# Kernel optimization log

Measured on AMD Instinct MI355X. Metric: run time of the kernel, lower is better.

## Reference

```python
import jax, jax.numpy as jnp
import numpy as np

B = 64
D = 4096          # width of every layer
# DAG: layer k consumes concat of prior layer outputs listed here (0 = input x)
CONNECTIONS = {1: [0], 2: [0, 1], 3: [1, 2], 4: [2, 3]}


def setup_inputs() -> dict:
    key = jax.random.key(0)
    keys = iter(jax.random.split(key, 32))
    inp = {"x": jax.random.normal(next(keys), (B, D), dtype=jnp.float32)}
    for k, v in CONNECTIONS.items():
        fan_in = D * len(v)
        bound = 1.0 / np.sqrt(fan_in)
        # kaiming_uniform_(a=sqrt(5)) -> U(-sqrt(6/((1+5)*fan_in)), +) = U(-1/sqrt(fan_in), +)
        inp[f"W{k}"] = jax.random.uniform(next(keys), (D, fan_in), jnp.float32, -bound, bound)
        inp[f"b{k}"] = jax.random.uniform(next(keys), (D,), jnp.float32, -bound, bound)
        # static binary mask (buffer in torch), stored as float like MaskedLinear expects
        inp[f"M{k}"] = (jax.random.uniform(next(keys), (D, fan_in)) < 0.5).astype(jnp.float32)
    return inp


def _dag_forward(x, Ws, bs, Ms):
    layer_output = [x]
    for k, v in CONNECTIONS.items():
        inputs = jnp.concatenate([layer_output[v_] for v_ in v], axis=1)  # [B, D*len(v)]
        # masked linear: y = inputs @ (W*M)^T + b, then ReLU
        y = jnp.einsum('bi,oi->bo', inputs, Ws[k] * Ms[k]) + bs[k]
        layer_output.append(jax.nn.relu(y))
    return layer_output[-1]


def reference(x, W1, b1, M1, W2, b2, M2, W3, b3, M3, W4, b4, M4):
    Ws = {1: W1, 2: W2, 3: W3, 4: W4}
    bs = {1: b1, 2: b2, 3: b3, 4: b4}
    Ms = {1: M1, 2: M2, 3: M3, 4: M4}
    return _dag_forward(x, Ws, bs, Ms)
```

## Files before the change

kernel.cpp:

```cpp
#include <hip/hip_runtime.h>
#include <hip/hip_bf16.h>
#include <stdint.h>


typedef __attribute__((ext_vector_type(8))) short  s8v;
typedef __attribute__((ext_vector_type(4))) float  f4v;
typedef __attribute__((ext_vector_type(2))) float  f2v;
typedef __attribute__((ext_vector_type(4))) unsigned short us4v;
typedef __attribute__((ext_vector_type(2))) unsigned short us2v;

#define LDA 16384
#define MFMA16 __builtin_amdgcn_mfma_f32_16x16x32_bf16

__device__ __forceinline__ short f2bf(float f) {
  unsigned int u = __builtin_bit_cast(unsigned int, f);
  u += 0x7fffu + ((u >> 16) & 1u);
  return (short)(u >> 16);
}
__device__ __forceinline__ float bf2f(short s) {
  unsigned int u = ((unsigned int)(unsigned short)s) << 16;
  return __builtin_bit_cast(float, u);
}

__global__ void dag_splitx(const float* __restrict__ x,
                           ushort* __restrict__ xh, ushort* __restrict__ xl) {
  int idx = blockIdx.x * blockDim.x + threadIdx.x;
  int m = idx >> 10;
  int n = (idx & 1023) << 2;
  f4v v = *(const f4v*)(x + (size_t)m * 4096 + n);
  us4v h, l;
#pragma unroll
  for (int j = 0; j < 4; ++j) {
    short hh = f2bf(v[j]);
    h[j] = (unsigned short)hh;
    l[j] = (unsigned short)f2bf(v[j] - bf2f(hh));
  }
  *(us4v*)(xh + (size_t)m * LDA + n) = h;
  *(us4v*)(xl + (size_t)m * LDA + n) = l;
}

struct RW { f4v w0a, w0b, w1a, w1b, m0a, m0b, m1a, m1b; };
struct RA { s8v ah0, ah1, ah2, ah3, al0, al1, al2, al3; };

template <int NSTEPS>
__global__ __launch_bounds__(256, 2) void dag_gemm_phaseA(
    const ushort* __restrict__ Ah,
    const ushort* __restrict__ Al,
    const float*  __restrict__ W,
    const float*  __restrict__ Mm,
    float*        __restrict__ partial,
    int K) {
  const int klen = NSTEPS * 32;
  const int tid  = threadIdx.x;
  const int wave = tid >> 6, lane = tid & 63;
  const int l15  = lane & 15, blk = lane >> 4;
  const int n0   = blockIdx.x * 128 + wave * 32;
  const int kbeg = blockIdx.y * klen;

  const float* wp0 = W  + (size_t)(n0 + l15) * K + kbeg + blk * 8;
  const float* wp1 = wp0 + (size_t)16 * K;
  const float* mp0 = Mm + (size_t)(n0 + l15) * K + kbeg + blk * 8;
  const float* mp1 = mp0 + (size_t)16 * K;
  const ushort* ap  = Ah + (size_t)l15 * LDA + kbeg + blk * 8;
  const ushort* alp = Al + (size_t)l15 * LDA + kbeg + blk * 8;

  f4v acc[4][2];
#pragma unroll
  for (int i = 0; i < 4; ++i) {
    acc[i][0] = (f4v){0.f, 0.f, 0.f, 0.f};
    acc[i][1] = (f4v){0.f, 0.f, 0.f, 0.f};
  }

  RW w[3];
  RA a[2];

  auto LOADW = [&](RW& r, int ko) {
    r.w0a = *(const f4v*)(wp0 + ko);     r.w0b = *(const f4v*)(wp0 + ko + 4);
    r.w1a = *(const f4v*)(wp1 + ko);     r.w1b = *(const f4v*)(wp1 + ko + 4);
    r.m0a = *(const f4v*)(mp0 + ko);     r.m0b = *(const f4v*)(mp0 + ko + 4);
    r.m1a = *(const f4v*)(mp1 + ko);     r.m1b = *(const f4v*)(mp1 + ko + 4);
  };
  auto LOADA = [&](RA& r, int ko) {
    r.ah0 = *(const s8v*)(ap  + ko);
    r.ah1 = *(const s8v*)(ap  + (size_t)16 * LDA + ko);
    r.ah2 = *(const s8v*)(ap  + (size_t)32 * LDA + ko);
    r.ah3 = *(const s8v*)(ap  + (size_t)48 * LDA + ko);
    r.al0 = *(const s8v*)(alp + ko);
    r.al1 = *(const s8v*)(alp + (size_t)16 * LDA + ko);
    r.al2 = *(const s8v*)(alp + (size_t)32 * LDA + ko);
    r.al3 = *(const s8v*)(alp + (size_t)48 * LDA + ko);
  };

  auto STEP = [&](RW& rw, RA& ra) {
    s8v wh0, wl0, wh1, wl1;
#pragma unroll
    for (int j = 0; j < 4; ++j) {
      { float ww = rw.w0a[j] * rw.m0a[j]; short h = f2bf(ww);
        wh0[j]     = h; wl0[j]     = f2bf(ww - bf2f(h)); }
      { float ww = rw.w0b[j] * rw.m0b[j]; short h = f2bf(ww);
        wh0[j + 4] = h; wl0[j + 4] = f2bf(ww - bf2f(h)); }
      { float ww = rw.w1a[j] * rw.m1a[j]; short h = f2bf(ww);
        wh1[j]     = h; wl1[j]     = f2bf(ww - bf2f(h)); }
      { float ww = rw.w1b[j] * rw.m1b[j]; short h = f2bf(ww);
        wh1[j + 4] = h; wl1[j + 4] = f2bf(ww - bf2f(h)); }
    }
    acc[0][0] = MFMA16(ra.ah0, wh0, acc[0][0], 0, 0, 0);
    acc[0][0] = MFMA16(ra.al0, wh0, acc[0][0], 0, 0, 0);
    acc[0][0] = MFMA16(ra.ah0, wl0, acc[0][0], 0, 0, 0);
    acc[1][0] = MFMA16(ra.ah1, wh0, acc[1][0], 0, 0, 0);
    acc[1][0] = MFMA16(ra.al1, wh0, acc[1][0], 0, 0, 0);
    acc[1][0] = MFMA16(ra.ah1, wl0, acc[1][0], 0, 0, 0);
    acc[2][0] = MFMA16(ra.ah2, wh0, acc[2][0], 0, 0, 0);
    acc[2][0] = MFMA16(ra.al2, wh0, acc[2][0], 0, 0, 0);
    acc[2][0] = MFMA16(ra.ah2, wl0, acc[2][0], 0, 0, 0);
    acc[3][0] = MFMA16(ra.ah3, wh0, acc[3][0], 0, 0, 0);
    acc[3][0] = MFMA16(ra.al3, wh0, acc[3][0], 0, 0, 0);
    acc[3][0] = MFMA16(ra.ah3, wl0, acc[3][0], 0, 0, 0);
    acc[0][1] = MFMA16(ra.ah0, wh1, acc[0][1], 0, 0, 0);
    acc[0][1] = MFMA16(ra.al0, wh1, acc[0][1], 0, 0, 0);
    acc[0][1] = MFMA16(ra.ah0, wl1, acc[0][1], 0, 0, 0);
    acc[1][1] = MFMA16(ra.ah1, wh1, acc[1][1], 0, 0, 0);
    acc[1][1] = MFMA16(ra.al1, wh1, acc[1][1], 0, 0, 0);
    acc[1][1] = MFMA16(ra.ah1, wl1, acc[1][1], 0, 0, 0);
    acc[2][1] = MFMA16(ra.ah2, wh1, acc[2][1], 0, 0, 0);
    acc[2][1] = MFMA16(ra.al2, wh1, acc[2][1], 0, 0, 0);
    acc[2][1] = MFMA16(ra.ah2, wl1, acc[2][1], 0, 0, 0);
    acc[3][1] = MFMA16(ra.ah3, wh1, acc[3][1], 0, 0, 0);
    acc[3][1] = MFMA16(ra.al3, wh1, acc[3][1], 0, 0, 0);
    acc[3][1] = MFMA16(ra.ah3, wl1, acc[3][1], 0, 0, 0);
  };

  LOADW(w[0], 0);
  if (NSTEPS > 1) LOADW(w[1], 32);
  LOADA(a[0], 0);
  if (NSTEPS > 1) LOADA(a[1], 32);

#pragma unroll
  for (int s = 0; s < NSTEPS; ++s) {
    if (s + 2 < NSTEPS) LOADW(w[(s + 2) % 3], (s + 2) * 32);
    STEP(w[s % 3], a[s & 1]);
    if (s + 2 < NSTEPS) LOADA(a[s & 1], (s + 2) * 32);
  }

  float* pout = partial + (size_t)blockIdx.y * (64 * 4096);
#pragma unroll
  for (int mt = 0; mt < 4; ++mt)
#pragma unroll
    for (int nt = 0; nt < 2; ++nt) {
      int n = n0 + nt * 16 + l15;
#pragma unroll
      for (int rr = 0; rr < 4; ++rr) {
        int m = mt * 16 + blk * 4 + rr;
        pout[(size_t)m * 4096 + n] = acc[mt][nt][rr];
      }
    }
}

__global__ void dag_phaseB(const float* __restrict__ partial, int splitk,
                           const float* __restrict__ bias,
                           ushort* __restrict__ yh, ushort* __restrict__ yl,
                           float* __restrict__ yf) {
  int idx = blockIdx.x * blockDim.x + threadIdx.x;
  int m = idx >> 11;
  int n = (idx & 2047) << 1;
  const float* p = partial + (size_t)m * 4096 + n;
  float s0 = 0.f, s1 = 0.f;
#pragma unroll 4
  for (int sp = 0; sp < splitk; ++sp) {
    f2v v = *(const f2v*)(p + (size_t)sp * (64 * 4096));
    s0 += v[0]; s1 += v[1];
  }
  const f2v bv = *(const f2v*)(bias + n);
  s0 = fmaxf(s0 + bv[0], 0.f);
  s1 = fmaxf(s1 + bv[1], 0.f);
  if (yf) {
    *(f2v*)(yf + (size_t)m * 4096 + n) = (f2v){s0, s1};
  } else {
    us2v h, l;
    short h0 = f2bf(s0); h[0] = (unsigned short)h0;
    l[0] = (unsigned short)f2bf(s0 - bf2f(h0));
    short h1 = f2bf(s1); h[1] = (unsigned short)h1;
    l[1] = (unsigned short)f2bf(s1 - bf2f(h1));
    *(us2v*)(yh + (size_t)m * LDA + n) = h;
    *(us2v*)(yl + (size_t)m * LDA + n) = l;
  }
}

extern "C" void kernel_launch(void* const* d_in, const int* in_sizes, int n_in,
                              void* d_out, int out_size, void* d_ws, size_t ws_size,
                              hipStream_t stream) {
  (void)in_sizes; (void)n_in; (void)out_size;
  const float* x = (const float*)d_in[0];
  struct L { const float *W, *b, *M; int K, incol, outcol; };
  L Ls[4] = {
      {(const float*)d_in[1],  (const float*)d_in[2],  (const float*)d_in[3],  4096, 0,    4096},
      {(const float*)d_in[4],  (const float*)d_in[5],  (const float*)d_in[6],  8192, 0,    8192},
      {(const float*)d_in[7],  (const float*)d_in[8],  (const float*)d_in[9],  8192, 4096, 12288},
      {(const float*)d_in[10], (const float*)d_in[11], (const float*)d_in[12], 8192, 8192, 16384},
  };
  float* out = (float*)d_out;

  char* ws = (char*)d_ws;
  ushort* Ah = (ushort*)ws;
  ushort* Al = (ushort*)(ws + (size_t)64 * LDA * 2);
  float* partial = (float*)(ws + (size_t)2 * 64 * LDA * 2);
  int SPLITK = 16;
  while (SPLITK > 1 &&
         ws_size < (size_t)4 * 1024 * 1024 + (size_t)SPLITK * 1024 * 1024)
    SPLITK >>= 1;

  dag_splitx<<<256, 256, 0, stream>>>(x, Ah, Al);

  for (int k = 0; k < 4; ++k) {
    dim3 grid(32, SPLITK);
    const ushort* Ahp = Ah + Ls[k].incol;
    const ushort* Alp = Al + Ls[k].incol;
    int nsteps = (Ls[k].K / SPLITK) / 32;
    switch (nsteps) {
      case 8:
        dag_gemm_phaseA<8><<<grid, 256, 0, stream>>>(
            Ahp, Alp, Ls[k].W, Ls[k].M, partial, Ls[k].K);
        break;
      case 16:
        dag_gemm_phaseA<16><<<grid, 256, 0, stream>>>(
            Ahp, Alp, Ls[k].W, Ls[k].M, partial, Ls[k].K);
        break;
      default:
        dag_gemm_phaseA<32><<<grid, 256, 0, stream>>>(
            Ahp, Alp, Ls[k].W, Ls[k].M, partial, Ls[k].K);
        break;
    }
    bool last = (k == 3);
    dag_phaseB<<<512, 256, 0, stream>>>(
        partial, SPLITK, Ls[k].b,
        last ? (ushort*)nullptr : Ah + Ls[k].outcol,
        last ? (ushort*)nullptr : Al + Ls[k].outcol,
        last ? out : (float*)nullptr);
  }
}
```

Measured before the change: 297.9 us.

## Stage weight and mask tiles through swizzled LDS with wider coalesced row loads

Weights and masks are no longer read straight into MFMA operand registers. Each wave now loads a 32-row by 64-column tile with 16 lanes covering one contiguous 256-byte row segment, writes it to a per-wave XOR-swizzled LDS region, and reads the MFMA fragments back from LDS. The aim is better global coalescing on the fp32 W and M streams, which dominate traffic. In exchange it adds LDS write and read traffic and 64 KB of dynamic shared memory per block, and the minimum split-K is raised to 4.

Result: faster. 280.9 us (-5.7%).

```diff
diff --git a/kernel.cpp b/kernel.cpp
--- a/kernel.cpp
+++ b/kernel.cpp
@@ -39,10 +39,9 @@
   *(us4v*)(xl + (size_t)m * LDA + n) = l;
 }
 
-struct RW { f4v w0a, w0b, w1a, w1b, m0a, m0b, m1a, m1b; };
 struct RA { s8v ah0, ah1, ah2, ah3, al0, al1, al2, al3; };
 
-template <int NSTEPS>
+template <int NSUPER>
 __global__ __launch_bounds__(256, 2) void dag_gemm_phaseA(
     const ushort* __restrict__ Ah,
     const ushort* __restrict__ Al,
@@ -50,35 +49,50 @@
     const float*  __restrict__ Mm,
     float*        __restrict__ partial,
     int K) {
-  const int klen = NSTEPS * 32;
+  extern __shared__ float smem[];
   const int tid  = threadIdx.x;
   const int wave = tid >> 6, lane = tid & 63;
   const int l15  = lane & 15, blk = lane >> 4;
   const int n0   = blockIdx.x * 128 + wave * 32;
+  const int klen = NSUPER * 64;
   const int kbeg = blockIdx.y * klen;
 
-  const float* wp0 = W  + (size_t)(n0 + l15) * K + kbeg + blk * 8;
-  const float* wp1 = wp0 + (size_t)16 * K;
-  const float* mp0 = Mm + (size_t)(n0 + l15) * K + kbeg + blk * 8;
-  const float* mp1 = mp0 + (size_t)16 * K;
+  float* WL = smem + wave * 4096;
+  float* ML = WL + 2048;
+
+  const int srow = lane >> 4;
+  const int sc   = lane & 15;
+
   const ushort* ap  = Ah + (size_t)l15 * LDA + kbeg + blk * 8;
   const ushort* alp = Al + (size_t)l15 * LDA + kbeg + blk * 8;
 
+  f4v stW[8], stM[8];
   f4v acc[4][2];
 #pragma unroll
   for (int i = 0; i < 4; ++i) {
     acc[i][0] = (f4v){0.f, 0.f, 0.f, 0.f};
     acc[i][1] = (f4v){0.f, 0.f, 0.f, 0.f};
   }
-
-  RW w[3];
-  RA a[2];
-
-  auto LOADW = [&](RW& r, int ko) {
-    r.w0a = *(const f4v*)(wp0 + ko);     r.w0b = *(const f4v*)(wp0 + ko + 4);
-    r.w1a = *(const f4v*)(wp1 + ko);     r.w1b = *(const f4v*)(wp1 + ko + 4);
-    r.m0a = *(const f4v*)(mp0 + ko);     r.m0b = *(const f4v*)(mp0 + ko + 4);
-    r.m1a = *(const f4v*)(mp1 + ko);     r.m1b = *(const f4v*)(mp1 + ko + 4);
+  RA a0, a1;
+
+  auto GLOAD = [&](int s) {
+    const float* wb = W  + (size_t)n0 * K + kbeg + s * 64 + sc * 4;
+    const float* mb = Mm + (size_t)n0 * K + kbeg + s * 64 + sc * 4;
+#pragma unroll
+    for (int j = 0; j < 8; ++j) {
+      size_t ro = (size_t)(4 * j + srow) * K;
+      stW[j] = *(const f4v*)(wb + ro);
+      stM[j] = *(const f4v*)(mb + ro);
+    }
+  };
+  auto DSWRITE = [&]() {
+#pragma unroll
+    for (int j = 0; j < 8; ++j) {
+      int row = 4 * j + srow;
+      int ci  = sc ^ (row & 15);
+      *(f4v*)(WL + row * 64 + ci * 4) = stW[j];
+      *(f4v*)(ML + row * 64 + ci * 4) = stM[j];
+    }
   };
   auto LOADA = [&](RA& r, int ko) {
     r.ah0 = *(const s8v*)(ap  + ko);
@@ -91,17 +105,28 @@
     r.al3 = *(const s8v*)(alp + (size_t)48 * LDA + ko);
   };
 
-  auto STEP = [&](RW& rw, RA& ra) {
+  auto KSTEP = [&](int kstep, RA& ra) {
+    const int cc = kstep * 8 + blk * 2;
+    const int c0 = cc ^ l15, c1 = (cc + 1) ^ l15;
+    const float* wr0 = WL + l15 * 64;
+    const float* wr1 = WL + (l15 + 16) * 64;
+    const float* mr0 = ML + l15 * 64;
+    const float* mr1 = ML + (l15 + 16) * 64;
+    f4v w0a = *(const f4v*)(wr0 + c0 * 4), w0b = *(const f4v*)(wr0 + c1 * 4);
+    f4v w1a = *(const f4v*)(wr1 + c0 * 4), w1b = *(const f4v*)(wr1 + c1 * 4);
+    f4v m0a = *(const f4v*)(mr0 + c0 * 4), m0b = *(const f4v*)(mr0 + c1 * 4);
+    f4v m1a = *(const f4v*)(mr1 + c0 * 4), m1b = *(const f4v*)(mr1 + c1 * 4);
+
     s8v wh0, wl0, wh1, wl1;
 #pragma unroll
     for (int j = 0; j < 4; ++j) {
-      { float ww = rw.w0a[j] * rw.m0a[j]; short h = f2bf(ww);
+      { float ww = w0a[j] * m0a[j]; short h = f2bf(ww);
         wh0[j]     = h; wl0[j]     = f2bf(ww - bf2f(h)); }
-      { float ww = rw.w0b[j] * rw.m0b[j]; short h = f2bf(ww);
+      { float ww = w0b[j] * m0b[j]; short h = f2bf(ww);
         wh0[j + 4] = h; wl0[j + 4] = f2bf(ww - bf2f(h)); }
-      { float ww = rw.w1a[j] * rw.m1a[j]; short h = f2bf(ww);
+      { float ww = w1a[j] * m1a[j]; short h = f2bf(ww);
         wh1[j]     = h; wl1[j]     = f2bf(ww - bf2f(h)); }
-      { float ww = rw.w1b[j] * rw.m1b[j]; short h = f2bf(ww);
+      { float ww = w1b[j] * m1b[j]; short h = f2bf(ww);
         wh1[j + 4] = h; wl1[j + 4] = f2bf(ww - bf2f(h)); }
     }
     acc[0][0] = MFMA16(ra.ah0, wh0, acc[0][0], 0, 0, 0);
@@ -130,16 +155,22 @@
     acc[3][1] = MFMA16(ra.ah3, wl1, acc[3][1], 0, 0, 0);
   };
 
-  LOADW(w[0], 0);
-  if (NSTEPS > 1) LOADW(w[1], 32);
-  LOADA(a[0], 0);
-  if (NSTEPS > 1) LOADA(a[1], 32);
-
-#pragma unroll
-  for (int s = 0; s < NSTEPS; ++s) {
-    if (s + 2 < NSTEPS) LOADW(w[(s + 2) % 3], (s + 2) * 32);
-    STEP(w[s % 3], a[s & 1]);
-    if (s + 2 < NSTEPS) LOADA(a[s & 1], (s + 2) * 32);
+  GLOAD(0);
+  DSWRITE();
+  if (NSUPER > 1) GLOAD(1);
+  LOADA(a0, 0);
+  LOADA(a1, 32);
+
+#pragma unroll
+  for (int s = 0; s < NSUPER; ++s) {
+    KSTEP(0, a0);
+    if (s + 1 < NSUPER) LOADA(a0, (s + 1) * 64);
+    KSTEP(1, a1);
+    if (s + 1 < NSUPER) LOADA(a1, (s + 1) * 64 + 32);
+    if (s + 1 < NSUPER) {
+      DSWRITE();
+      if (s + 2 < NSUPER) GLOAD(s + 2);
+    }
   }
 
   float* pout = partial + (size_t)blockIdx.y * (64 * 4096);
@@ -205,28 +236,29 @@
   ushort* Al = (ushort*)(ws + (size_t)64 * LDA * 2);
   float* partial = (float*)(ws + (size_t)2 * 64 * LDA * 2);
   int SPLITK = 16;
-  while (SPLITK > 1 &&
+  while (SPLITK > 4 &&
          ws_size < (size_t)4 * 1024 * 1024 + (size_t)SPLITK * 1024 * 1024)
     SPLITK >>= 1;
 
   dag_splitx<<<256, 256, 0, stream>>>(x, Ah, Al);
 
+  const size_t smem = 65536;
   for (int k = 0; k < 4; ++k) {
     dim3 grid(32, SPLITK);
     const ushort* Ahp = Ah + Ls[k].incol;
     const ushort* Alp = Al + Ls[k].incol;
-    int nsteps = (Ls[k].K / SPLITK) / 32;
-    switch (nsteps) {
-      case 8:
-        dag_gemm_phaseA<8><<<grid, 256, 0, stream>>>(
+    int nsuper = (Ls[k].K / SPLITK) / 64;
+    switch (nsuper) {
+      case 4:
+        dag_gemm_phaseA<4><<<grid, 256, smem, stream>>>(
             Ahp, Alp, Ls[k].W, Ls[k].M, partial, Ls[k].K);
         break;
-      case 16:
-        dag_gemm_phaseA<16><<<grid, 256, 0, stream>>>(
+      case 8:
+        dag_gemm_phaseA<8><<<grid, 256, smem, stream>>>(
             Ahp, Alp, Ls[k].W, Ls[k].M, partial, Ls[k].K);
         break;
       default:
-        dag_gemm_phaseA<32><<<grid, 256, 0, stream>>>(
+        dag_gemm_phaseA<16><<<grid, 256, smem, stream>>>(
             Ahp, Alp, Ls[k].W, Ls[k].M, partial, Ls[k].K);
         break;
     }
```
